# Optimization experiments

Hardware: AMD Instinct MI355X
Metric: run time of the kernel (lower is better)

## Reference

```python
import jax, jax.numpy as jnp
import numpy as np

NUM_NODES = 2048   # N (spatial)
SEQ_LEN = 512      # T (temporal)
LATENT = 32
LAYERS = 2
SELF_LOOP_EPS = 0.5
B = 4


def setup_inputs() -> dict:
    key = jax.random.key(0)
    k1, k2, k3 = jax.random.split(key, 3)
    NT = NUM_NODES + SEQ_LEN
    X = jax.random.normal(k1, (B, NT, LATENT), dtype=jnp.float32)
    # GraphSAGE-style per-layer weights: self and neighbor transforms + bias
    Ws = jax.random.normal(k2, (LAYERS, LATENT, LATENT), dtype=jnp.float32) * 0.05
    Wn = jax.random.normal(k3, (LAYERS, LATENT, LATENT), dtype=jnp.float32) * 0.05
    b = jnp.zeros((LAYERS, LATENT), dtype=jnp.float32)
    return {"X": X, "Ws": Ws, "Wn": Wn, "b": b}


def build_adj(X):
    # node_embs = concat(spatial, temporal) == X itself
    adj = jnp.einsum('bnf,bmf->bnm', X, X)          # [B, N+T, N+T]
    adj = jnp.tanh(jax.nn.relu(adj))
    NT = X.shape[1]
    adj = adj + SELF_LOOP_EPS * jnp.eye(NT, dtype=adj.dtype)
    return adj


def reference(X, Ws, Wn, b):
    adj = build_adj(X)
    h = X
    # dense weighted aggregation == sparse message passing over nonzero edges,
    # since edge weights are exactly the adjacency values
    for l in range(LAYERS):
        agg = jnp.einsum('bnm,bmd->bnd', adj, h)    # neighbor aggregation
        h = jax.nn.elu(jnp.einsum('bnd,de->bne', h, Ws[l])
                       + jnp.einsum('bnd,de->bne', agg, Wn[l])
                       + b[l])
    return h
```

## Files before the change

### kernel.cpp

```cpp
#include <hip/hip_runtime.h>
#include <math.h>

#define NT 2560
#define DF 32
#define NB 4
#define SELF_EPS 0.5f
#define MS 8
#define MROWS (NT / MS)
#define MT 64
#define MITERS (MROWS / MT)
#define TN 64

typedef __attribute__((ext_vector_type(8))) short bf16x8;
typedef __attribute__((ext_vector_type(4))) float f32x4;

__device__ __forceinline__ unsigned short f2bf(float f) {
    unsigned u = __builtin_bit_cast(unsigned, f);
    u += 0x7fffu + ((u >> 16) & 1u);
    return (unsigned short)(u >> 16);
}

__device__ __forceinline__ float fast_rcp(float x) {
#if __has_builtin(__builtin_amdgcn_rcpf)
    return __builtin_amdgcn_rcpf(x);
#else
    return 1.0f / x;
#endif
}

__device__ __forceinline__ float tanh_relu(float x) {
    x = fmaxf(x, 0.0f);
    float e = __expf(x + x);
    return 1.0f - 2.0f * fast_rcp(e + 1.0f);
}

__global__ __launch_bounds__(256, 4)
void prep(const float* __restrict__ X, float* __restrict__ aggz,
          unsigned short* __restrict__ Xb, unsigned short* __restrict__ XT)
{
    const int bid = blockIdx.x, t = threadIdx.x;
    if (bid < 640) {
        f32x4 z = {0.f, 0.f, 0.f, 0.f};
        ((f32x4*)aggz)[(size_t)bid * 256 + t] = z;
        return;
    }
    __shared__ float sT[32][33];
    const int tile = bid - 640;
    const int b = tile / 80, n0 = (tile % 80) * 32;
    const int row = t >> 3, c4 = (t & 7) * 4;
    const size_t rbase = ((size_t)(b * NT + n0 + row)) * DF + c4;
    const float4 v = *(const float4*)(X + rbase);
    unsigned p0 = (unsigned)f2bf(v.x) | ((unsigned)f2bf(v.y) << 16);
    unsigned p1 = (unsigned)f2bf(v.z) | ((unsigned)f2bf(v.w) << 16);
    *(uint2*)(Xb + rbase) = make_uint2(p0, p1);
    sT[row][c4 + 0] = v.x; sT[row][c4 + 1] = v.y;
    sT[row][c4 + 2] = v.z; sT[row][c4 + 3] = v.w;
    __syncthreads();
    const int d = t >> 3, nq = (t & 7) * 4;
    unsigned q0 = (unsigned)f2bf(sT[nq + 0][d]) | ((unsigned)f2bf(sT[nq + 1][d]) << 16);
    unsigned q1 = (unsigned)f2bf(sT[nq + 2][d]) | ((unsigned)f2bf(sT[nq + 3][d]) << 16);
    *(uint2*)(XT + ((size_t)(b * DF + d)) * NT + n0 + nq) = make_uint2(q0, q1);
}

__global__ __launch_bounds__(256, 4)
void gsage_main(const unsigned short* __restrict__ Xb,
                const unsigned short* __restrict__ HT,
                float* __restrict__ agg)
{
    __shared__ unsigned short XmL[64 * 40];
    __shared__ unsigned short HtL[32 * 72];
    __shared__ unsigned short Ss[4 * 16 * 72];

    const int t = threadIdx.x;
    const int w = t >> 6, lane = t & 63;
    const int q = lane >> 4, c = lane & 15;
    const int n0 = blockIdx.x * TN;
    const int mbase = blockIdx.y * MROWS;
    const int b = blockIdx.z;

    const size_t xbase = (size_t)b * NT * DF;
    const size_t tbase = (size_t)b * DF * NT;

    const bf16x8 bfn = *(const bf16x8*)(Xb + xbase + (size_t)(n0 + w * 16 + c) * DF + q * 8);

    f32x4 acc0 = {0.f, 0.f, 0.f, 0.f};
    f32x4 acc1 = {0.f, 0.f, 0.f, 0.f};

    const int xrow = t >> 2, xseg = t & 3;
    const int hrow = t >> 3, hseg = t & 7;

    uint4 xv = *(const uint4*)(Xb + xbase + (size_t)(mbase + xrow) * DF + xseg * 8);
    uint4 hv = *(const uint4*)(HT + tbase + (size_t)hrow * NT + mbase + hseg * 8);

    const int n_g = n0 + w * 16 + c;
    unsigned short* SsW = Ss + w * (16 * 72);

    for (int it = 0; it < MITERS; ++it) {
        const int m0 = mbase + it * MT;
        __syncthreads();
        *(uint4*)(XmL + xrow * 40 + xseg * 8) = xv;
        *(uint4*)(HtL + hrow * 72 + hseg * 8) = hv;
        if (it + 1 < MITERS) {
            const int m1 = m0 + MT;
            xv = *(const uint4*)(Xb + xbase + (size_t)(m1 + xrow) * DF + xseg * 8);
            hv = *(const uint4*)(HT + tbase + (size_t)hrow * NT + m1 + hseg * 8);
        }
        __syncthreads();

        #pragma unroll
        for (int t4 = 0; t4 < 4; ++t4) {
            const bf16x8 af = *(const bf16x8*)(XmL + (t4 * 16 + c) * 40 + q * 8);
            const f32x4 zero = {0.f, 0.f, 0.f, 0.f};
            f32x4 st = __builtin_amdgcn_mfma_f32_16x16x32_bf16(af, bfn, zero, 0, 0, 0);
            const int m2 = m0 + t4 * 16 + q * 4;
            float v0 = tanh_relu(st[0]); if (n_g == m2 + 0) v0 += SELF_EPS;
            float v1 = tanh_relu(st[1]); if (n_g == m2 + 1) v1 += SELF_EPS;
            float v2 = tanh_relu(st[2]); if (n_g == m2 + 2) v2 += SELF_EPS;
            float v3 = tanh_relu(st[3]); if (n_g == m2 + 3) v3 += SELF_EPS;
            unsigned p0 = (unsigned)f2bf(v0) | ((unsigned)f2bf(v1) << 16);
            unsigned p1 = (unsigned)f2bf(v2) | ((unsigned)f2bf(v3) << 16);
            *(uint2*)(SsW + c * 72 + t4 * 16 + q * 4) = make_uint2(p0, p1);
        }
        asm volatile("s_waitcnt lgkmcnt(0)" ::: "memory");

        #pragma unroll
        for (int kc = 0; kc < 2; ++kc) {
            const bf16x8 sf = *(const bf16x8*)(SsW + c * 72 + kc * 32 + q * 8);
            const bf16x8 h0 = *(const bf16x8*)(HtL + c * 72 + kc * 32 + q * 8);
            const bf16x8 h1 = *(const bf16x8*)(HtL + (16 + c) * 72 + kc * 32 + q * 8);
            acc0 = __builtin_amdgcn_mfma_f32_16x16x32_bf16(sf, h0, acc0, 0, 0, 0);
            acc1 = __builtin_amdgcn_mfma_f32_16x16x32_bf16(sf, h1, acc1, 0, 0, 0);
        }
    }

    float* ap = agg + xbase + (size_t)(n0 + w * 16 + q * 4) * DF + c;
    #pragma unroll
    for (int r = 0; r < 4; ++r) {
        atomicAdd(ap + (size_t)r * DF, acc0[r]);
        atomicAdd(ap + (size_t)r * DF + 16, acc1[r]);
    }
}

__global__ __launch_bounds__(256, 4)
void gsage_epi(const float* __restrict__ Hin, const float* __restrict__ agg,
               const float* __restrict__ Wsl, const float* __restrict__ Wnl,
               const float* __restrict__ bl,
               float* __restrict__ Hout, unsigned short* __restrict__ HTout)
{
    __shared__ float sW[32][33], sN[32][33], sH[32][36], sA[32][36], sT[32][33];
    const int t = threadIdx.x;
    const int n0 = blockIdx.x * 32;
    const int b = blockIdx.y;
    const int row = t >> 3, c4 = (t & 7) * 4;
    const size_t rb = ((size_t)(b * NT + n0 + row)) * DF + c4;
    const float4 hv = *(const float4*)(Hin + rb);
    const float4 av = *(const float4*)(agg + rb);
    const float4 w0 = *(const float4*)(Wsl + row * DF + c4);
    const float4 w1 = *(const float4*)(Wnl + row * DF + c4);
    sH[row][c4+0]=hv.x; sH[row][c4+1]=hv.y; sH[row][c4+2]=hv.z; sH[row][c4+3]=hv.w;
    sA[row][c4+0]=av.x; sA[row][c4+1]=av.y; sA[row][c4+2]=av.z; sA[row][c4+3]=av.w;
    sW[row][c4+0]=w0.x; sW[row][c4+1]=w0.y; sW[row][c4+2]=w0.z; sW[row][c4+3]=w0.w;
    sN[row][c4+0]=w1.x; sN[row][c4+1]=w1.y; sN[row][c4+2]=w1.z; sN[row][c4+3]=w1.w;
    __syncthreads();

    float4 z = make_float4(bl[c4+0], bl[c4+1], bl[c4+2], bl[c4+3]);
    #pragma unroll
    for (int k = 0; k < DF; ++k) {
        const float hk = sH[row][k], ak = sA[row][k];
        z.x += hk * sW[k][c4+0] + ak * sN[k][c4+0];
        z.y += hk * sW[k][c4+1] + ak * sN[k][c4+1];
        z.z += hk * sW[k][c4+2] + ak * sN[k][c4+2];
        z.w += hk * sW[k][c4+3] + ak * sN[k][c4+3];
    }
    z.x = z.x > 0.f ? z.x : __expf(z.x) - 1.f;
    z.y = z.y > 0.f ? z.y : __expf(z.y) - 1.f;
    z.z = z.z > 0.f ? z.z : __expf(z.z) - 1.f;
    z.w = z.w > 0.f ? z.w : __expf(z.w) - 1.f;
    *(float4*)(Hout + rb) = z;

    if (HTout != nullptr) {
        sT[row][c4+0]=z.x; sT[row][c4+1]=z.y; sT[row][c4+2]=z.z; sT[row][c4+3]=z.w;
        __syncthreads();
        const int d = t >> 3, nq = (t & 7) * 4;
        unsigned q0 = (unsigned)f2bf(sT[nq+0][d]) | ((unsigned)f2bf(sT[nq+1][d]) << 16);
        unsigned q1 = (unsigned)f2bf(sT[nq+2][d]) | ((unsigned)f2bf(sT[nq+3][d]) << 16);
        *(uint2*)(HTout + ((size_t)(b * DF + d)) * NT + n0 + nq) = make_uint2(q0, q1);
    }
}

extern "C" void kernel_launch(void* const* d_in, const int* in_sizes, int n_in,
                              void* d_out, int out_size, void* d_ws, size_t ws_size,
                              hipStream_t stream) {
    const float* X  = (const float*)d_in[0];
    const float* Ws = (const float*)d_in[1];
    const float* Wn = (const float*)d_in[2];
    const float* bv = (const float*)d_in[3];
    float* out = (float*)d_out;

    char* ws = (char*)d_ws;
    float* agg1 = (float*)ws;
    float* agg2 = agg1 + (size_t)NB * NT * DF;
    float* h1   = agg2 + (size_t)NB * NT * DF;
    unsigned short* Xb  = (unsigned short*)(ws + 3932160);
    unsigned short* XT  = Xb + (size_t)NB * NT * DF;
    unsigned short* H1T = XT + (size_t)NB * NT * DF;

    prep<<<960, 256, 0, stream>>>(X, agg1, Xb, XT);

    dim3 g(NT / TN, MS, NB);
    gsage_main<<<g, 256, 0, stream>>>(Xb, XT, agg1);
    gsage_epi<<<dim3(NT / 32, NB), 256, 0, stream>>>(X, agg1, Ws, Wn, bv, h1, H1T);
    gsage_main<<<g, 256, 0, stream>>>(Xb, H1T, agg2);
    gsage_epi<<<dim3(NT / 32, NB), 256, 0, stream>>>(h1, agg2, Ws + DF * DF, Wn + DF * DF,
                                                     bv + DF, out, nullptr);
}
```

Before: 102.1 us.

## Replace atomic aggregation with per-split partial buffers reduced in epilogue

The main kernel now writes its partial aggregation for each m-split into a separate slice of a buffer with plain stores, instead of doing atomicAdd into a buffer zeroed beforehand. The epilogue sums the eight partial slices. This removes the zeroing blocks from prep and avoids atomic contention. A second change splits the diagonal check into its own branch so only tiles containing the diagonal pay for the self-loop comparisons. The cost is a larger workspace and eight times more aggregation reads in the epilogue.

```diff
diff --git a/kernel.cpp b/kernel.cpp
--- a/kernel.cpp
+++ b/kernel.cpp
@@ -35,17 +35,12 @@
 }
 
 __global__ __launch_bounds__(256, 4)
-void prep(const float* __restrict__ X, float* __restrict__ aggz,
+void prep(const float* __restrict__ X,
           unsigned short* __restrict__ Xb, unsigned short* __restrict__ XT)
 {
-    const int bid = blockIdx.x, t = threadIdx.x;
-    if (bid < 640) {
-        f32x4 z = {0.f, 0.f, 0.f, 0.f};
-        ((f32x4*)aggz)[(size_t)bid * 256 + t] = z;
-        return;
-    }
+    const int t = threadIdx.x;
     __shared__ float sT[32][33];
-    const int tile = bid - 640;
+    const int tile = blockIdx.x;
     const int b = tile / 80, n0 = (tile % 80) * 32;
     const int row = t >> 3, c4 = (t & 7) * 4;
     const size_t rbase = ((size_t)(b * NT + n0 + row)) * DF + c4;
@@ -65,7 +60,7 @@
 __global__ __launch_bounds__(256, 4)
 void gsage_main(const unsigned short* __restrict__ Xb,
                 const unsigned short* __restrict__ HT,
-                float* __restrict__ agg)
+                float* __restrict__ P)
 {
     __shared__ unsigned short XmL[64 * 40];
     __shared__ unsigned short HtL[32 * 72];
@@ -107,19 +102,35 @@
         }
         __syncthreads();
 
-        #pragma unroll
-        for (int t4 = 0; t4 < 4; ++t4) {
-            const bf16x8 af = *(const bf16x8*)(XmL + (t4 * 16 + c) * 40 + q * 8);
-            const f32x4 zero = {0.f, 0.f, 0.f, 0.f};
-            f32x4 st = __builtin_amdgcn_mfma_f32_16x16x32_bf16(af, bfn, zero, 0, 0, 0);
-            const int m2 = m0 + t4 * 16 + q * 4;
-            float v0 = tanh_relu(st[0]); if (n_g == m2 + 0) v0 += SELF_EPS;
-            float v1 = tanh_relu(st[1]); if (n_g == m2 + 1) v1 += SELF_EPS;
-            float v2 = tanh_relu(st[2]); if (n_g == m2 + 2) v2 += SELF_EPS;
-            float v3 = tanh_relu(st[3]); if (n_g == m2 + 3) v3 += SELF_EPS;
-            unsigned p0 = (unsigned)f2bf(v0) | ((unsigned)f2bf(v1) << 16);
-            unsigned p1 = (unsigned)f2bf(v2) | ((unsigned)f2bf(v3) << 16);
-            *(uint2*)(SsW + c * 72 + t4 * 16 + q * 4) = make_uint2(p0, p1);
+        if (m0 == n0) {
+            #pragma unroll
+            for (int t4 = 0; t4 < 4; ++t4) {
+                const bf16x8 af = *(const bf16x8*)(XmL + (t4 * 16 + c) * 40 + q * 8);
+                const f32x4 zero = {0.f, 0.f, 0.f, 0.f};
+                f32x4 st = __builtin_amdgcn_mfma_f32_16x16x32_bf16(af, bfn, zero, 0, 0, 0);
+                const int m2 = m0 + t4 * 16 + q * 4;
+                float v0 = tanh_relu(st[0]); if (n_g == m2 + 0) v0 += SELF_EPS;
+                float v1 = tanh_relu(st[1]); if (n_g == m2 + 1) v1 += SELF_EPS;
+                float v2 = tanh_relu(st[2]); if (n_g == m2 + 2) v2 += SELF_EPS;
+                float v3 = tanh_relu(st[3]); if (n_g == m2 + 3) v3 += SELF_EPS;
+                unsigned p0 = (unsigned)f2bf(v0) | ((unsigned)f2bf(v1) << 16);
+                unsigned p1 = (unsigned)f2bf(v2) | ((unsigned)f2bf(v3) << 16);
+                *(uint2*)(SsW + c * 72 + t4 * 16 + q * 4) = make_uint2(p0, p1);
+            }
+        } else {
+            #pragma unroll
+            for (int t4 = 0; t4 < 4; ++t4) {
+                const bf16x8 af = *(const bf16x8*)(XmL + (t4 * 16 + c) * 40 + q * 8);
+                const f32x4 zero = {0.f, 0.f, 0.f, 0.f};
+                f32x4 st = __builtin_amdgcn_mfma_f32_16x16x32_bf16(af, bfn, zero, 0, 0, 0);
+                float v0 = tanh_relu(st[0]);
+                float v1 = tanh_relu(st[1]);
+                float v2 = tanh_relu(st[2]);
+                float v3 = tanh_relu(st[3]);
+                unsigned p0 = (unsigned)f2bf(v0) | ((unsigned)f2bf(v1) << 16);
+                unsigned p1 = (unsigned)f2bf(v2) | ((unsigned)f2bf(v3) << 16);
+                *(uint2*)(SsW + c * 72 + t4 * 16 + q * 4) = make_uint2(p0, p1);
+            }
         }
         asm volatile("s_waitcnt lgkmcnt(0)" ::: "memory");
 
@@ -133,16 +144,17 @@
         }
     }
 
-    float* ap = agg + xbase + (size_t)(n0 + w * 16 + q * 4) * DF + c;
+    float* ap = P + ((size_t)blockIdx.y * NB + b) * NT * DF
+                  + (size_t)(n0 + w * 16 + q * 4) * DF + c;
     #pragma unroll
     for (int r = 0; r < 4; ++r) {
-        atomicAdd(ap + (size_t)r * DF, acc0[r]);
-        atomicAdd(ap + (size_t)r * DF + 16, acc1[r]);
+        ap[(size_t)r * DF] = acc0[r];
+        ap[(size_t)r * DF + 16] = acc1[r];
     }
 }
 
 __global__ __launch_bounds__(256, 4)
-void gsage_epi(const float* __restrict__ Hin, const float* __restrict__ agg,
+void gsage_epi(const float* __restrict__ Hin, const float* __restrict__ P,
                const float* __restrict__ Wsl, const float* __restrict__ Wnl,
                const float* __restrict__ bl,
                float* __restrict__ Hout, unsigned short* __restrict__ HTout)
@@ -154,7 +166,13 @@
     const int row = t >> 3, c4 = (t & 7) * 4;
     const size_t rb = ((size_t)(b * NT + n0 + row)) * DF + c4;
     const float4 hv = *(const float4*)(Hin + rb);
-    const float4 av = *(const float4*)(agg + rb);
+    const size_t pstride = (size_t)NB * NT * DF;
+    float4 av = *(const float4*)(P + rb);
+    #pragma unroll
+    for (int s = 1; s < MS; ++s) {
+        const float4 pv = *(const float4*)(P + (size_t)s * pstride + rb);
+        av.x += pv.x; av.y += pv.y; av.z += pv.z; av.w += pv.w;
+    }
     const float4 w0 = *(const float4*)(Wsl + row * DF + c4);
     const float4 w1 = *(const float4*)(Wnl + row * DF + c4);
     sH[row][c4+0]=hv.x; sH[row][c4+1]=hv.y; sH[row][c4+2]=hv.z; sH[row][c4+3]=hv.w;
@@ -198,19 +216,18 @@
     float* out = (float*)d_out;
 
     char* ws = (char*)d_ws;
-    float* agg1 = (float*)ws;
-    float* agg2 = agg1 + (size_t)NB * NT * DF;
-    float* h1   = agg2 + (size_t)NB * NT * DF;
-    unsigned short* Xb  = (unsigned short*)(ws + 3932160);
+    float* P  = (float*)ws;
+    float* h1 = P + (size_t)MS * NB * NT * DF;
+    unsigned short* Xb  = (unsigned short*)(ws + 11796480);
     unsigned short* XT  = Xb + (size_t)NB * NT * DF;
     unsigned short* H1T = XT + (size_t)NB * NT * DF;
 
-    prep<<<960, 256, 0, stream>>>(X, agg1, Xb, XT);
+    prep<<<320, 256, 0, stream>>>(X, Xb, XT);
 
     dim3 g(NT / TN, MS, NB);
-    gsage_main<<<g, 256, 0, stream>>>(Xb, XT, agg1);
-    gsage_epi<<<dim3(NT / 32, NB), 256, 0, stream>>>(X, agg1, Ws, Wn, bv, h1, H1T);
-    gsage_main<<<g, 256, 0, stream>>>(Xb, H1T, agg2);
-    gsage_epi<<<dim3(NT / 32, NB), 256, 0, stream>>>(h1, agg2, Ws + DF * DF, Wn + DF * DF,
+    gsage_main<<<g, 256, 0, stream>>>(Xb, XT, P);
+    gsage_epi<<<dim3(NT / 32, NB), 256, 0, stream>>>(X, P, Ws, Wn, bv, h1, H1T);
+    gsage_main<<<g, 256, 0, stream>>>(Xb, H1T, P);
+    gsage_epi<<<dim3(NT / 32, NB), 256, 0, stream>>>(h1, P, Ws + DF * DF, Wn + DF * DF,
                                                      bv + DF, out, nullptr);
 }
```

After: 106.4 us. 1.04x slower.

## Cache bf16 adjacency fragments and fuse aggregation with epilogue per row block

Applied to the files above, without the earlier changes.

The first layer kernel now writes the computed tanh-relu adjacency tiles in MFMA fragment layout to global memory. The second layer reuses them instead of recomputing the similarity GEMM and tanh. Each block owns 16 output rows and splits the m-range across 4 waves with an LDS reduction, which removes the float atomics, the zero-init pass and the separate epilogue kernels. The cost is a large adjacency buffer write and read (about 52 MB in bf16) and fewer, smaller blocks.

```diff
diff --git a/kernel.cpp b/kernel.cpp
--- a/kernel.cpp
+++ b/kernel.cpp
@@ -5,11 +5,13 @@
 #define DF 32
 #define NB 4
 #define SELF_EPS 0.5f
-#define MS 8
-#define MROWS (NT / MS)
+#define WMS 4
+#define MROWS (NT / WMS)
 #define MT 64
 #define MITERS (MROWS / MT)
-#define TN 64
+#define TN 16
+#define NBK (NT / TN)
+#define SG_FRAG (MITERS * 2 * 64 * 8)
 
 typedef __attribute__((ext_vector_type(8))) short bf16x8;
 typedef __attribute__((ext_vector_type(4))) float f32x4;
@@ -35,17 +37,12 @@
 }
 
 __global__ __launch_bounds__(256, 4)
-void prep(const float* __restrict__ X, float* __restrict__ aggz,
+void prep(const float* __restrict__ X,
           unsigned short* __restrict__ Xb, unsigned short* __restrict__ XT)
 {
-    const int bid = blockIdx.x, t = threadIdx.x;
-    if (bid < 640) {
-        f32x4 z = {0.f, 0.f, 0.f, 0.f};
-        ((f32x4*)aggz)[(size_t)bid * 256 + t] = z;
-        return;
-    }
+    const int t = threadIdx.x;
     __shared__ float sT[32][33];
-    const int tile = bid - 640;
+    const int tile = blockIdx.x;
     const int b = tile / 80, n0 = (tile % 80) * 32;
     const int row = t >> 3, c4 = (t & 7) * 4;
     const size_t rbase = ((size_t)(b * NT + n0 + row)) * DF + c4;
@@ -62,129 +59,289 @@
     *(uint2*)(XT + ((size_t)(b * DF + d)) * NT + n0 + nq) = make_uint2(q0, q1);
 }
 
-__global__ __launch_bounds__(256, 4)
-void gsage_main(const unsigned short* __restrict__ Xb,
-                const unsigned short* __restrict__ HT,
-                float* __restrict__ agg)
+union K1LDS {
+    struct {
+        unsigned short Xm[WMS][64 * 40];
+        unsigned short Ht[WMS][32 * 72];
+        unsigned short Ss[WMS][16 * 72];
+    } m;
+    struct {
+        float red[WMS][16][32];
+        float sW[32][33], sN[32][33];
+        float sH[16][33], sA[16][33], sT[16][33];
+    } e;
+};
+
+__global__ __launch_bounds__(256, 3)
+void k1(const float* __restrict__ X,
+        const unsigned short* __restrict__ Xb,
+        const unsigned short* __restrict__ XT,
+        const float* __restrict__ Wsl, const float* __restrict__ Wnl,
+        const float* __restrict__ bl,
+        float* __restrict__ h1, unsigned short* __restrict__ H1T,
+        unsigned short* __restrict__ Sg)
 {
-    __shared__ unsigned short XmL[64 * 40];
-    __shared__ unsigned short HtL[32 * 72];
-    __shared__ unsigned short Ss[4 * 16 * 72];
-
+    __shared__ K1LDS L;
     const int t = threadIdx.x;
     const int w = t >> 6, lane = t & 63;
     const int q = lane >> 4, c = lane & 15;
-    const int n0 = blockIdx.x * TN;
-    const int mbase = blockIdx.y * MROWS;
-    const int b = blockIdx.z;
-
+    const int nb = blockIdx.x, b = blockIdx.y;
+    const int n0 = nb * TN;
     const size_t xbase = (size_t)b * NT * DF;
     const size_t tbase = (size_t)b * DF * NT;
-
-    const bf16x8 bfn = *(const bf16x8*)(Xb + xbase + (size_t)(n0 + w * 16 + c) * DF + q * 8);
+    const int mw = w * MROWS;
+
+    const bf16x8 bfn = *(const bf16x8*)(Xb + xbase + (size_t)(n0 + c) * DF + q * 8);
+
+    const int xrow = lane >> 2, xseg = lane & 3;
+    const int hrow = lane >> 3, hseg = lane & 7;
+
+    uint4 xv[4], hv[4];
+#pragma unroll
+    for (int s = 0; s < 4; ++s) {
+        xv[s] = *(const uint4*)(Xb + xbase + (size_t)(mw + s * 16 + xrow) * DF + xseg * 8);
+        hv[s] = *(const uint4*)(XT + tbase + (size_t)(s * 8 + hrow) * NT + mw + hseg * 8);
+    }
+
+    unsigned short* XmW = L.m.Xm[w];
+    unsigned short* HtW = L.m.Ht[w];
+    unsigned short* SsW = L.m.Ss[w];
+    unsigned short* Sgw = Sg + (((size_t)b * NBK + nb) * WMS + w) * SG_FRAG
+                        + (size_t)lane * 8;
 
     f32x4 acc0 = {0.f, 0.f, 0.f, 0.f};
     f32x4 acc1 = {0.f, 0.f, 0.f, 0.f};
 
-    const int xrow = t >> 2, xseg = t & 3;
-    const int hrow = t >> 3, hseg = t & 7;
-
-    uint4 xv = *(const uint4*)(Xb + xbase + (size_t)(mbase + xrow) * DF + xseg * 8);
-    uint4 hv = *(const uint4*)(HT + tbase + (size_t)hrow * NT + mbase + hseg * 8);
-
-    const int n_g = n0 + w * 16 + c;
-    unsigned short* SsW = Ss + w * (16 * 72);
-
     for (int it = 0; it < MITERS; ++it) {
-        const int m0 = mbase + it * MT;
-        __syncthreads();
-        *(uint4*)(XmL + xrow * 40 + xseg * 8) = xv;
-        *(uint4*)(HtL + hrow * 72 + hseg * 8) = hv;
+        const int m0 = mw + it * MT;
+        asm volatile("s_waitcnt lgkmcnt(0)" ::: "memory");
+#pragma unroll
+        for (int s = 0; s < 4; ++s) {
+            *(uint4*)(XmW + (s * 16 + xrow) * 40 + xseg * 8) = xv[s];
+            *(uint4*)(HtW + (s * 8 + hrow) * 72 + hseg * 8) = hv[s];
+        }
         if (it + 1 < MITERS) {
             const int m1 = m0 + MT;
-            xv = *(const uint4*)(Xb + xbase + (size_t)(m1 + xrow) * DF + xseg * 8);
-            hv = *(const uint4*)(HT + tbase + (size_t)hrow * NT + m1 + hseg * 8);
-        }
-        __syncthreads();
-
-        #pragma unroll
+#pragma unroll
+            for (int s = 0; s < 4; ++s) {
+                xv[s] = *(const uint4*)(Xb + xbase + (size_t)(m1 + s * 16 + xrow) * DF + xseg * 8);
+                hv[s] = *(const uint4*)(XT + tbase + (size_t)(s * 8 + hrow) * NT + m1 + hseg * 8);
+            }
+        }
+        asm volatile("s_waitcnt lgkmcnt(0)" ::: "memory");
+
+#pragma unroll
         for (int t4 = 0; t4 < 4; ++t4) {
-            const bf16x8 af = *(const bf16x8*)(XmL + (t4 * 16 + c) * 40 + q * 8);
+            const bf16x8 af = *(const bf16x8*)(XmW + (t4 * 16 + c) * 40 + q * 8);
             const f32x4 zero = {0.f, 0.f, 0.f, 0.f};
             f32x4 st = __builtin_amdgcn_mfma_f32_16x16x32_bf16(af, bfn, zero, 0, 0, 0);
-            const int m2 = m0 + t4 * 16 + q * 4;
-            float v0 = tanh_relu(st[0]); if (n_g == m2 + 0) v0 += SELF_EPS;
-            float v1 = tanh_relu(st[1]); if (n_g == m2 + 1) v1 += SELF_EPS;
-            float v2 = tanh_relu(st[2]); if (n_g == m2 + 2) v2 += SELF_EPS;
-            float v3 = tanh_relu(st[3]); if (n_g == m2 + 3) v3 += SELF_EPS;
+            const int mt = m0 + t4 * 16;
+            float v0 = tanh_relu(st[0]), v1 = tanh_relu(st[1]);
+            float v2 = tanh_relu(st[2]), v3 = tanh_relu(st[3]);
+            if ((unsigned)(n0 - mt) < 16u || (unsigned)(mt - n0) < 16u) {
+                const int m2 = mt + q * 4, n_g = n0 + c;
+                if (n_g == m2 + 0) v0 += SELF_EPS;
+                if (n_g == m2 + 1) v1 += SELF_EPS;
+                if (n_g == m2 + 2) v2 += SELF_EPS;
+                if (n_g == m2 + 3) v3 += SELF_EPS;
+            }
             unsigned p0 = (unsigned)f2bf(v0) | ((unsigned)f2bf(v1) << 16);
             unsigned p1 = (unsigned)f2bf(v2) | ((unsigned)f2bf(v3) << 16);
             *(uint2*)(SsW + c * 72 + t4 * 16 + q * 4) = make_uint2(p0, p1);
         }
         asm volatile("s_waitcnt lgkmcnt(0)" ::: "memory");
 
-        #pragma unroll
+#pragma unroll
         for (int kc = 0; kc < 2; ++kc) {
             const bf16x8 sf = *(const bf16x8*)(SsW + c * 72 + kc * 32 + q * 8);
-            const bf16x8 h0 = *(const bf16x8*)(HtL + c * 72 + kc * 32 + q * 8);
-            const bf16x8 h1 = *(const bf16x8*)(HtL + (16 + c) * 72 + kc * 32 + q * 8);
-            acc0 = __builtin_amdgcn_mfma_f32_16x16x32_bf16(sf, h0, acc0, 0, 0, 0);
-            acc1 = __builtin_amdgcn_mfma_f32_16x16x32_bf16(sf, h1, acc1, 0, 0, 0);
-        }
-    }
-
-    float* ap = agg + xbase + (size_t)(n0 + w * 16 + q * 4) * DF + c;
-    #pragma unroll
+            *(uint4*)(Sgw + (size_t)(it * 2 + kc) * (64 * 8)) = __builtin_bit_cast(uint4, sf);
+            const bf16x8 hf0 = *(const bf16x8*)(HtW + c * 72 + kc * 32 + q * 8);
+            const bf16x8 hf1 = *(const bf16x8*)(HtW + (16 + c) * 72 + kc * 32 + q * 8);
+            acc0 = __builtin_amdgcn_mfma_f32_16x16x32_bf16(sf, hf0, acc0, 0, 0, 0);
+            acc1 = __builtin_amdgcn_mfma_f32_16x16x32_bf16(sf, hf1, acc1, 0, 0, 0);
+        }
+    }
+
+    asm volatile("s_waitcnt lgkmcnt(0)" ::: "memory");
+    __syncthreads();
+
+#pragma unroll
     for (int r = 0; r < 4; ++r) {
-        atomicAdd(ap + (size_t)r * DF, acc0[r]);
-        atomicAdd(ap + (size_t)r * DF + 16, acc1[r]);
-    }
-}
+        L.e.red[w][q * 4 + r][c]      = acc0[r];
+        L.e.red[w][q * 4 + r][16 + c] = acc1[r];
+    }
+    const int row8 = t >> 3, c4 = (t & 7) * 4;
+    {
+        const float4 wv0 = *(const float4*)(Wsl + row8 * DF + c4);
+        const float4 wv1 = *(const float4*)(Wnl + row8 * DF + c4);
+        L.e.sW[row8][c4+0]=wv0.x; L.e.sW[row8][c4+1]=wv0.y;
+        L.e.sW[row8][c4+2]=wv0.z; L.e.sW[row8][c4+3]=wv0.w;
+        L.e.sN[row8][c4+0]=wv1.x; L.e.sN[row8][c4+1]=wv1.y;
+        L.e.sN[row8][c4+2]=wv1.z; L.e.sN[row8][c4+3]=wv1.w;
+    }
+    float4 hvv;
+    if (t < 128) {
+        hvv = *(const float4*)(X + xbase + (size_t)(n0 + row8) * DF + c4);
+    }
+    __syncthreads();
+    if (t < 128) {
+        float4 a = *(const float4*)&L.e.red[0][row8][c4];
+#pragma unroll
+        for (int ww = 1; ww < WMS; ++ww) {
+            const float4 p = *(const float4*)&L.e.red[ww][row8][c4];
+            a.x += p.x; a.y += p.y; a.z += p.z; a.w += p.w;
+        }
+        L.e.sA[row8][c4+0]=a.x; L.e.sA[row8][c4+1]=a.y;
+        L.e.sA[row8][c4+2]=a.z; L.e.sA[row8][c4+3]=a.w;
+        L.e.sH[row8][c4+0]=hvv.x; L.e.sH[row8][c4+1]=hvv.y;
+        L.e.sH[row8][c4+2]=hvv.z; L.e.sH[row8][c4+3]=hvv.w;
+    }
+    __syncthreads();
+    if (t < 128) {
+        float4 z = make_float4(bl[c4+0], bl[c4+1], bl[c4+2], bl[c4+3]);
+#pragma unroll
+        for (int k = 0; k < DF; ++k) {
+            const float hk = L.e.sH[row8][k], ak = L.e.sA[row8][k];
+            z.x += hk * L.e.sW[k][c4+0] + ak * L.e.sN[k][c4+0];
+            z.y += hk * L.e.sW[k][c4+1] + ak * L.e.sN[k][c4+1];
+            z.z += hk * L.e.sW[k][c4+2] + ak * L.e.sN[k][c4+2];
+            z.w += hk * L.e.sW[k][c4+3] + ak * L.e.sN[k][c4+3];
+        }
+        z.x = z.x > 0.f ? z.x : __expf(z.x) - 1.f;
+        z.y = z.y > 0.f ? z.y : __expf(z.y) - 1.f;
+        z.z = z.z > 0.f ? z.z : __expf(z.z) - 1.f;
+        z.w = z.w > 0.f ? z.w : __expf(z.w) - 1.f;
+        *(float4*)(h1 + xbase + (size_t)(n0 + row8) * DF + c4) = z;
+        L.e.sT[row8][c4+0]=z.x; L.e.sT[row8][c4+1]=z.y;
+        L.e.sT[row8][c4+2]=z.z; L.e.sT[row8][c4+3]=z.w;
+    }
+    __syncthreads();
+    if (t < 128) {
+        const int d = t >> 2, seg = t & 3;
+        unsigned r0 = (unsigned)f2bf(L.e.sT[seg*4+0][d]) | ((unsigned)f2bf(L.e.sT[seg*4+1][d]) << 16);
+        unsigned r1 = (unsigned)f2bf(L.e.sT[seg*4+2][d]) | ((unsigned)f2bf(L.e.sT[seg*4+3][d]) << 16);
+        *(uint2*)(H1T + tbase + (size_t)d * NT + n0 + seg * 4) = make_uint2(r0, r1);
+    }
+}
+
+union K2LDS {
+    struct { unsigned short Ht[WMS][32 * 72]; } m;
+    struct {
+        float red[WMS][16][32];
+        float sW[32][33], sN[32][33];
+        float sH[16][33], sA[16][33];
+    } e;
+};
 
 __global__ __launch_bounds__(256, 4)
-void gsage_epi(const float* __restrict__ Hin, const float* __restrict__ agg,
-               const float* __restrict__ Wsl, const float* __restrict__ Wnl,
-               const float* __restrict__ bl,
-               float* __restrict__ Hout, unsigned short* __restrict__ HTout)
+void k2(const float* __restrict__ Hin, const unsigned short* __restrict__ HT,
+        const unsigned short* __restrict__ Sg,
+        const float* __restrict__ Wsl, const float* __restrict__ Wnl,
+        const float* __restrict__ bl, float* __restrict__ out)
 {
-    __shared__ float sW[32][33], sN[32][33], sH[32][36], sA[32][36], sT[32][33];
+    __shared__ K2LDS L;
     const int t = threadIdx.x;
-    const int n0 = blockIdx.x * 32;
-    const int b = blockIdx.y;
-    const int row = t >> 3, c4 = (t & 7) * 4;
-    const size_t rb = ((size_t)(b * NT + n0 + row)) * DF + c4;
-    const float4 hv = *(const float4*)(Hin + rb);
-    const float4 av = *(const float4*)(agg + rb);
-    const float4 w0 = *(const float4*)(Wsl + row * DF + c4);
-    const float4 w1 = *(const float4*)(Wnl + row * DF + c4);
-    sH[row][c4+0]=hv.x; sH[row][c4+1]=hv.y; sH[row][c4+2]=hv.z; sH[row][c4+3]=hv.w;
-    sA[row][c4+0]=av.x; sA[row][c4+1]=av.y; sA[row][c4+2]=av.z; sA[row][c4+3]=av.w;
-    sW[row][c4+0]=w0.x; sW[row][c4+1]=w0.y; sW[row][c4+2]=w0.z; sW[row][c4+3]=w0.w;
-    sN[row][c4+0]=w1.x; sN[row][c4+1]=w1.y; sN[row][c4+2]=w1.z; sN[row][c4+3]=w1.w;
-    __syncthreads();
-
-    float4 z = make_float4(bl[c4+0], bl[c4+1], bl[c4+2], bl[c4+3]);
-    #pragma unroll
-    for (int k = 0; k < DF; ++k) {
-        const float hk = sH[row][k], ak = sA[row][k];
-        z.x += hk * sW[k][c4+0] + ak * sN[k][c4+0];
-        z.y += hk * sW[k][c4+1] + ak * sN[k][c4+1];
-        z.z += hk * sW[k][c4+2] + ak * sN[k][c4+2];
-        z.w += hk * sW[k][c4+3] + ak * sN[k][c4+3];
-    }
-    z.x = z.x > 0.f ? z.x : __expf(z.x) - 1.f;
-    z.y = z.y > 0.f ? z.y : __expf(z.y) - 1.f;
-    z.z = z.z > 0.f ? z.z : __expf(z.z) - 1.f;
-    z.w = z.w > 0.f ? z.w : __expf(z.w) - 1.f;
-    *(float4*)(Hout + rb) = z;
-
-    if (HTout != nullptr) {
-        sT[row][c4+0]=z.x; sT[row][c4+1]=z.y; sT[row][c4+2]=z.z; sT[row][c4+3]=z.w;
-        __syncthreads();
-        const int d = t >> 3, nq = (t & 7) * 4;
-        unsigned q0 = (unsigned)f2bf(sT[nq+0][d]) | ((unsigned)f2bf(sT[nq+1][d]) << 16);
-        unsigned q1 = (unsigned)f2bf(sT[nq+2][d]) | ((unsigned)f2bf(sT[nq+3][d]) << 16);
-        *(uint2*)(HTout + ((size_t)(b * DF + d)) * NT + n0 + nq) = make_uint2(q0, q1);
+    const int w = t >> 6, lane = t & 63;
+    const int q = lane >> 4, c = lane & 15;
+    const int nb = blockIdx.x, b = blockIdx.y;
+    const int n0 = nb * TN;
+    const size_t xbase = (size_t)b * NT * DF;
+    const size_t tbase = (size_t)b * DF * NT;
+    const int mw = w * MROWS;
+
+    const int hrow = lane >> 3, hseg = lane & 7;
+    uint4 hv[4];
+#pragma unroll
+    for (int s = 0; s < 4; ++s)
+        hv[s] = *(const uint4*)(HT + tbase + (size_t)(s * 8 + hrow) * NT + mw + hseg * 8);
+
+    const unsigned short* Sp = Sg + (((size_t)b * NBK + nb) * WMS + w) * SG_FRAG
+                             + (size_t)lane * 8;
+    bf16x8 sf0 = *(const bf16x8*)(Sp);
+    bf16x8 sf1 = *(const bf16x8*)(Sp + 512);
+
+    unsigned short* HtW = L.m.Ht[w];
+    f32x4 acc0 = {0.f, 0.f, 0.f, 0.f};
+    f32x4 acc1 = {0.f, 0.f, 0.f, 0.f};
+
+    for (int it = 0; it < MITERS; ++it) {
+        asm volatile("s_waitcnt lgkmcnt(0)" ::: "memory");
+#pragma unroll
+        for (int s = 0; s < 4; ++s)
+            *(uint4*)(HtW + (s * 8 + hrow) * 72 + hseg * 8) = hv[s];
+        bf16x8 nsf0, nsf1;
+        if (it + 1 < MITERS) {
+            const int m1 = mw + (it + 1) * MT;
+#pragma unroll
+            for (int s = 0; s < 4; ++s)
+                hv[s] = *(const uint4*)(HT + tbase + (size_t)(s * 8 + hrow) * NT + m1 + hseg * 8);
+            nsf0 = *(const bf16x8*)(Sp + (size_t)(it + 1) * 1024);
+            nsf1 = *(const bf16x8*)(Sp + (size_t)(it + 1) * 1024 + 512);
+        }
+        asm volatile("s_waitcnt lgkmcnt(0)" ::: "memory");
+
+        const bf16x8 h00 = *(const bf16x8*)(HtW + c * 72 + q * 8);
+        const bf16x8 h01 = *(const bf16x8*)(HtW + (16 + c) * 72 + q * 8);
+        acc0 = __builtin_amdgcn_mfma_f32_16x16x32_bf16(sf0, h00, acc0, 0, 0, 0);
+        acc1 = __builtin_amdgcn_mfma_f32_16x16x32_bf16(sf0, h01, acc1, 0, 0, 0);
+        const bf16x8 h10 = *(const bf16x8*)(HtW + c * 72 + 32 + q * 8);
+        const bf16x8 h11 = *(const bf16x8*)(HtW + (16 + c) * 72 + 32 + q * 8);
+        acc0 = __builtin_amdgcn_mfma_f32_16x16x32_bf16(sf1, h10, acc0, 0, 0, 0);
+        acc1 = __builtin_amdgcn_mfma_f32_16x16x32_bf16(sf1, h11, acc1, 0, 0, 0);
+
+        if (it + 1 < MITERS) { sf0 = nsf0; sf1 = nsf1; }
+    }
+
+    asm volatile("s_waitcnt lgkmcnt(0)" ::: "memory");
+    __syncthreads();
+
+#pragma unroll
+    for (int r = 0; r < 4; ++r) {
+        L.e.red[w][q * 4 + r][c]      = acc0[r];
+        L.e.red[w][q * 4 + r][16 + c] = acc1[r];
+    }
+    const int row8 = t >> 3, c4 = (t & 7) * 4;
+    {
+        const float4 wv0 = *(const float4*)(Wsl + row8 * DF + c4);
+        const float4 wv1 = *(const float4*)(Wnl + row8 * DF + c4);
+        L.e.sW[row8][c4+0]=wv0.x; L.e.sW[row8][c4+1]=wv0.y;
+        L.e.sW[row8][c4+2]=wv0.z; L.e.sW[row8][c4+3]=wv0.w;
+        L.e.sN[row8][c4+0]=wv1.x; L.e.sN[row8][c4+1]=wv1.y;
+        L.e.sN[row8][c4+2]=wv1.z; L.e.sN[row8][c4+3]=wv1.w;
+    }
+    float4 hvv;
+    if (t < 128) {
+        hvv = *(const float4*)(Hin + xbase + (size_t)(n0 + row8) * DF + c4);
+    }
+    __syncthreads();
+    if (t < 128) {
+        float4 a = *(const float4*)&L.e.red[0][row8][c4];
+#pragma unroll
+        for (int ww = 1; ww < WMS; ++ww) {
+            const float4 p = *(const float4*)&L.e.red[ww][row8][c4];
+            a.x += p.x; a.y += p.y; a.z += p.z; a.w += p.w;
+        }
+        L.e.sA[row8][c4+0]=a.x; L.e.sA[row8][c4+1]=a.y;
+        L.e.sA[row8][c4+2]=a.z; L.e.sA[row8][c4+3]=a.w;
+        L.e.sH[row8][c4+0]=hvv.x; L.e.sH[row8][c4+1]=hvv.y;
+        L.e.sH[row8][c4+2]=hvv.z; L.e.sH[row8][c4+3]=hvv.w;
+    }
+    __syncthreads();
+    if (t < 128) {
+        float4 z = make_float4(bl[c4+0], bl[c4+1], bl[c4+2], bl[c4+3]);
+#pragma unroll
+        for (int k = 0; k < DF; ++k) {
+            const float hk = L.e.sH[row8][k], ak = L.e.sA[row8][k];
+            z.x += hk * L.e.sW[k][c4+0] + ak * L.e.sN[k][c4+0];
+            z.y += hk * L.e.sW[k][c4+1] + ak * L.e.sN[k][c4+1];
+            z.z += hk * L.e.sW[k][c4+2] + ak * L.e.sN[k][c4+2];
+            z.w += hk * L.e.sW[k][c4+3] + ak * L.e.sN[k][c4+3];
+        }
+        z.x = z.x > 0.f ? z.x : __expf(z.x) - 1.f;
+        z.y = z.y > 0.f ? z.y : __expf(z.y) - 1.f;
+        z.z = z.z > 0.f ? z.z : __expf(z.z) - 1.f;
+        z.w = z.w > 0.f ? z.w : __expf(z.w) - 1.f;
+        *(float4*)(out + xbase + (size_t)(n0 + row8) * DF + c4) = z;
     }
 }
 
@@ -198,19 +355,14 @@
     float* out = (float*)d_out;
 
     char* ws = (char*)d_ws;
-    float* agg1 = (float*)ws;
-    float* agg2 = agg1 + (size_t)NB * NT * DF;
-    float* h1   = agg2 + (size_t)NB * NT * DF;
-    unsigned short* Xb  = (unsigned short*)(ws + 3932160);
+    float* h1 = (float*)ws;
+    unsigned short* Xb  = (unsigned short*)(ws + 1310720);
     unsigned short* XT  = Xb + (size_t)NB * NT * DF;
     unsigned short* H1T = XT + (size_t)NB * NT * DF;
-
-    prep<<<960, 256, 0, stream>>>(X, agg1, Xb, XT);
-
-    dim3 g(NT / TN, MS, NB);
-    gsage_main<<<g, 256, 0, stream>>>(Xb, XT, agg1);
-    gsage_epi<<<dim3(NT / 32, NB), 256, 0, stream>>>(X, agg1, Ws, Wn, bv, h1, H1T);
-    gsage_main<<<g, 256, 0, stream>>>(Xb, H1T, agg2);
-    gsage_epi<<<dim3(NT / 32, NB), 256, 0, stream>>>(h1, agg2, Ws + DF * DF, Wn + DF * DF,
-                                                     bv + DF, out, nullptr);
-}
+    unsigned short* Sg  = H1T + (size_t)NB * NT * DF;
+
+    prep<<<320, 256, 0, stream>>>(X, Xb, XT);
+    k1<<<dim3(NBK, NB), 256, 0, stream>>>(X, Xb, XT, Ws, Wn, bv, h1, H1T, Sg);
+    k2<<<dim3(NBK, NB), 256, 0, stream>>>(h1, H1T, Sg, Ws + DF * DF, Wn + DF * DF,
+                                          bv + DF, out);
+}
```

Measured after the change: 169.5 us. +66.0%, slower.
